# Kernel tuning notes

Hardware: AMD Instinct MI355X
Metric: run time of the kernel (lower is better)

Reference implementation:

```python
import jax, jax.numpy as jnp
import numpy as np

N = 8192
E = 262144
DIN = 512
DOUT = 256


def setup_inputs() -> dict:
    key = jax.random.key(0)
    k1, k2, k3, k4 = jax.random.split(key, 4)
    x = jax.random.normal(k1, (N, DIN), dtype=jnp.float32)
    edge_index = jax.random.randint(k2, (2, E), 0, N, dtype=jnp.int64)
    edge_weight = jax.random.uniform(k3, (E,), dtype=jnp.float32)
    W = jax.random.normal(k4, (DOUT, DIN), dtype=jnp.float32) * (1.0 / np.sqrt(DIN))
    return {"x": x, "edge_index": edge_index, "edge_weight": edge_weight, "W": W}


def reference(x, edge_index, edge_weight, W):
    n = x.shape[0]
    # Linear(dim_in, dim_out, bias=False): h = x @ W.T  -> [N, DOUT]
    h = x @ W.T
    # Dense adjacency: A[src, dst] += w (to_dense_adj sums duplicate edges)
    src, dst = edge_index[0], edge_index[1]
    A = jnp.zeros((n, n), dtype=x.dtype).at[src, dst].add(edge_weight)
    # degree from A BEFORE self-loops, then +1 from the added eye on degree_matrix
    deg = jnp.sum(A, axis=1) + 1.0
    # sqrt(inverse(diag(deg))) == diag(1/sqrt(deg)); apply as row scaling
    dinv_sqrt = 1.0 / jnp.sqrt(deg)  # [N]
    A = A + jnp.eye(n, dtype=x.dtype)  # self-loops on adjacency
    # x = D^{-1/2} @ (A.T @ (D^{-1/2} @ h))
    h = dinv_sqrt[:, None] * h
    h = A.T @ h
    h = dinv_sqrt[:, None] * h
    return h
```

## Files before the change

kernel.cpp:

```cpp
#include <hip/hip_runtime.h>

static constexpr int DIN = 512;
static constexpr int DOUT = 256;
static constexpr int NR = 8;
static constexpr int SLOT = 24;
static constexpr int EPT = 4;
static constexpr float DEG_SCALE = 1048576.0f;
static constexpr float DEG_INV = 1.0f / 1048576.0f;

typedef __attribute__((ext_vector_type(8))) short short8;
typedef __attribute__((ext_vector_type(4))) float f32x4;
typedef __attribute__((ext_vector_type(2))) unsigned int u32x2;
typedef __attribute__((ext_vector_type(4))) unsigned int u32x4;

__device__ inline unsigned short f2bf(float f) {
  unsigned int b = __float_as_uint(f);
  unsigned int r = (b + 0x7fffu + ((b >> 16) & 1u)) >> 16;
  return (unsigned short)r;
}
__device__ inline float bf_lo(unsigned int packed) { return __uint_as_float(packed << 16); }
__device__ inline float bf_hi(unsigned int packed) { return __uint_as_float(packed & 0xffff0000u); }

__device__ inline short8 cvt8(const f32x4 a, const f32x4 b) {
  short8 o;
  o[0] = (short)f2bf(a[0]); o[1] = (short)f2bf(a[1]);
  o[2] = (short)f2bf(a[2]); o[3] = (short)f2bf(a[3]);
  o[4] = (short)f2bf(b[0]); o[5] = (short)f2bf(b[1]);
  o[6] = (short)f2bf(b[2]); o[7] = (short)f2bf(b[3]);
  return o;
}

__device__ inline int xcd_id() {
  int v;
  asm volatile("s_getreg_b32 %0, hwreg(20)" : "=s"(v));
  return v & (NR - 1);
}

__global__ __launch_bounds__(256) void k_prep(
    const float* __restrict__ W, unsigned short* __restrict__ wbb,
    int* __restrict__ dz, int nz, int wgroups) {
  const int gid = blockIdx.x * 256 + threadIdx.x;
  if (gid < nz) dz[gid] = 0;
  const int wi = gid - nz;
  if (wi >= 0 && wi < wgroups) {
    const f32x4* src = (const f32x4*)(W + (size_t)wi * 8);
    f32x4 a = src[0], b = src[1];
    *(short8*)(wbb + (size_t)wi * 8) = cvt8(a, b);
  }
}

__global__ __launch_bounds__(256) void k_edges(
    const int* __restrict__ ei, const float* __restrict__ ew,
    int* __restrict__ degi_rep, int* __restrict__ cursor_rep,
    uint2* __restrict__ bucket, int n, int E) {
  const int x = xcd_id();
  int* __restrict__ degr = degi_rep + (size_t)x * n;
  int* __restrict__ curr = cursor_rep + (size_t)x * n;
  const int e0 = blockIdx.x * 256 * EPT + threadIdx.x;
  int sv[EPT], dv[EPT], wq[EPT];
  float wf[EPT];
#pragma unroll
  for (int u = 0; u < EPT; ++u) {
    const int e = min(e0 + u * 256, E - 1);
    sv[u] = __builtin_nontemporal_load(ei + e);
    dv[u] = __builtin_nontemporal_load(ei + E + e);
    wf[u] = __builtin_nontemporal_load(ew + e);
    wq[u] = __float2int_rn(wf[u] * DEG_SCALE);
  }
  const bool live = (e0 + (EPT - 1) * 256) < E;
#pragma unroll
  for (int u = 0; u < EPT; ++u)
    if (live || e0 + u * 256 < E) atomicAdd(&degr[sv[u]], wq[u]);
  int pos[EPT];
#pragma unroll
  for (int u = 0; u < EPT; ++u)
    pos[u] = (live || e0 + u * 256 < E) ? atomicAdd(&curr[dv[u]], 1) : SLOT;
#pragma unroll
  for (int u = 0; u < EPT; ++u) {
    if (pos[u] < SLOT) {
      u32x2 v;
      v[0] = (unsigned)sv[u];
      v[1] = __float_as_uint(wf[u]);
      __builtin_nontemporal_store(
          v, (u32x2*)(bucket + ((size_t)dv[u] * NR + x) * SLOT + pos[u]));
    }
  }
}

__global__ __launch_bounds__(256) void k_gemm(
    const float* __restrict__ x, const unsigned short* __restrict__ wbb,
    const int* __restrict__ degi_rep, float* __restrict__ sdeg,
    unsigned short* __restrict__ h1b, int n) {
  if (blockIdx.x < (n >> 8)) {
    const int i = blockIdx.x * 256 + threadIdx.x;
    int sum = 0;
#pragma unroll
    for (int r = 0; r < NR; ++r) sum += degi_rep[(size_t)r * n + i];
    sdeg[i] = __frsqrt_rn(1.0f + (float)sum * DEG_INV);
  }
  const int lane = threadIdx.x & 63;
  const int wv = threadIdx.x >> 6;
  const int bm = blockIdx.x * 16;
  const int colb = wv * 64;
  const int r = lane & 15;
  const int kg = lane >> 4;
  f32x4 acc[4] = {};
  const float* arow = x + (size_t)(bm + r) * DIN + kg * 8;
  const unsigned short* brow0 = wbb + (size_t)(colb + r) * DIN + kg * 8;
#pragma unroll
  for (int k0 = 0; k0 < DIN; k0 += 32) {
    f32x4 a0 = *(const f32x4*)(arow + k0);
    f32x4 a1 = *(const f32x4*)(arow + k0 + 4);
    short8 av = cvt8(a0, a1);
#pragma unroll
    for (int nt = 0; nt < 4; ++nt) {
      short8 bv = *(const short8*)(brow0 + (size_t)nt * 16 * DIN + k0);
      acc[nt] = __builtin_amdgcn_mfma_f32_16x16x32_bf16(av, bv, acc[nt], 0, 0, 0);
    }
  }
#pragma unroll
  for (int i = 0; i < 4; ++i) {
    int row = bm + kg * 4 + i;
#pragma unroll
    for (int nt = 0; nt < 4; ++nt) {
      h1b[(size_t)row * DOUT + colb + nt * 16 + r] = f2bf(acc[nt][i]);
    }
  }
}

__global__ __launch_bounds__(256, 4) void k_gather(
    const unsigned short* __restrict__ h1b, const float* __restrict__ sdeg,
    const int* __restrict__ cursor_rep, const uint2* __restrict__ bucket,
    float* __restrict__ out, int n) {
  const int lane = threadIdx.x & 63;
  const int wv = threadIdx.x >> 6;
  const int dst = blockIdx.x * 4 + wv;
  const int cl = lane & 31;
  const int half = lane >> 5;

  int pre[NR + 1];
  pre[0] = 0;
#pragma unroll
  for (int r = 0; r < NR; ++r) {
    int c = min(cursor_rep[(size_t)r * n + dst], SLOT);
    pre[r + 1] = pre[r] + c;
  }
  const int cnt = pre[NR];

  const u32x4 selfv = *(const u32x4*)(h1b + (size_t)dst * DOUT + cl * 8);
  const float sd = sdeg[dst];

  float acc[8] = {};

  for (int base = 0; base < cnt; base += 64) {
    const int c = min(64, cnt - base);
    int sv = 0;
    float wl = 0.f;
    if (lane < c) {
      const int g = base + lane;
      int rr = 0;
#pragma unroll
      for (int r = 1; r < NR; ++r) rr += (g >= pre[r]) ? 1 : 0;
      const int slot = g - pre[rr];
      u32x2 ev = __builtin_nontemporal_load(
          (const u32x2*)(bucket + ((size_t)dst * NR + rr) * SLOT + slot));
      sv = (int)ev[0];
      wl = __uint_as_float(ev[1]) * sdeg[sv];
    }
    const int npair = ((c + 15) >> 4) << 3;
    for (int j = 0; j < npair; j += 8) {
      u32x4 rbuf[8];
#pragma unroll
      for (int u = 0; u < 8; ++u) {
        int src = __shfl(sv, 2 * (j + u) + half);
        rbuf[u] = *(const u32x4*)(h1b + (size_t)src * DOUT + cl * 8);
      }
#pragma unroll
      for (int u = 0; u < 8; ++u) {
        float w = __shfl(wl, 2 * (j + u) + half);
        acc[0] = fmaf(w, bf_lo(rbuf[u][0]), acc[0]);
        acc[1] = fmaf(w, bf_hi(rbuf[u][0]), acc[1]);
        acc[2] = fmaf(w, bf_lo(rbuf[u][1]), acc[2]);
        acc[3] = fmaf(w, bf_hi(rbuf[u][1]), acc[3]);
        acc[4] = fmaf(w, bf_lo(rbuf[u][2]), acc[4]);
        acc[5] = fmaf(w, bf_hi(rbuf[u][2]), acc[5]);
        acc[6] = fmaf(w, bf_lo(rbuf[u][3]), acc[6]);
        acc[7] = fmaf(w, bf_hi(rbuf[u][3]), acc[7]);
      }
    }
  }

#pragma unroll
  for (int k = 0; k < 8; ++k) acc[k] += __shfl_xor(acc[k], 32);

  if (half == 0) {
    f32x4 o0v, o1v;
    o0v[0] = sd * fmaf(sd, bf_lo(selfv[0]), acc[0]);
    o0v[1] = sd * fmaf(sd, bf_hi(selfv[0]), acc[1]);
    o0v[2] = sd * fmaf(sd, bf_lo(selfv[1]), acc[2]);
    o0v[3] = sd * fmaf(sd, bf_hi(selfv[1]), acc[3]);
    o1v[0] = sd * fmaf(sd, bf_lo(selfv[2]), acc[4]);
    o1v[1] = sd * fmaf(sd, bf_hi(selfv[2]), acc[5]);
    o1v[2] = sd * fmaf(sd, bf_lo(selfv[3]), acc[6]);
    o1v[3] = sd * fmaf(sd, bf_hi(selfv[3]), acc[7]);
    float* op = out + (size_t)dst * DOUT + cl * 8;
    __builtin_nontemporal_store(o0v, (f32x4*)op);
    __builtin_nontemporal_store(o1v, (f32x4*)(op + 4));
  }
}

extern "C" void kernel_launch(void* const* d_in, const int* in_sizes, int n_in,
                              void* d_out, int out_size, void* d_ws, size_t ws_size,
                              hipStream_t stream) {
  const float* x = (const float*)d_in[0];
  const int* ei = (const int*)d_in[1];
  const float* ew = (const float*)d_in[2];
  const float* W = (const float*)d_in[3];
  float* out = (float*)d_out;

  const int n = in_sizes[0] / DIN;
  const int E = in_sizes[2];

  char* p = (char*)d_ws;
  auto alloc = [&](size_t bytes) {
    char* q = p;
    p += (bytes + 255) & ~(size_t)255;
    return q;
  };
  unsigned short* h1b = (unsigned short*)alloc((size_t)n * DOUT * 2);
  unsigned short* wbb = (unsigned short*)alloc((size_t)DOUT * DIN * 2);
  int* degi_rep   = (int*)alloc((size_t)NR * n * 4);
  int* cursor_rep = (int*)alloc((size_t)NR * n * 4);
  float* sdeg     = (float*)alloc((size_t)n * 4);
  uint2* bucket   = (uint2*)alloc((size_t)n * NR * SLOT * 8);

  const int nz = 2 * NR * n;
  const int wgroups = DOUT * DIN / 8;
  const int prep_blocks = (nz + wgroups + 255) / 256;
  const int edge_blocks = (E + 256 * EPT - 1) / (256 * EPT);

  k_prep<<<prep_blocks, 256, 0, stream>>>(W, wbb, degi_rep, nz, wgroups);
  k_edges<<<edge_blocks, 256, 0, stream>>>(ei, ew, degi_rep, cursor_rep, bucket, n, E);
  k_gemm<<<n / 16, 256, 0, stream>>>(x, wbb, degi_rep, sdeg, h1b, n);
  k_gather<<<n / 4, 256, 0, stream>>>(h1b, sdeg, cursor_rep, bucket, out, n);
}
```

Measured before the change: 77.12 us.

## Bin edges per segment with LDS histograms instead of global replicated atomics

```diff
diff --git a/kernel.cpp b/kernel.cpp
--- a/kernel.cpp
+++ b/kernel.cpp
@@ -2,9 +2,10 @@
 
 static constexpr int DIN = 512;
 static constexpr int DOUT = 256;
-static constexpr int NR = 8;
-static constexpr int SLOT = 24;
-static constexpr int EPT = 4;
+static constexpr int NB = 8;
+static constexpr int SEG = 32768;
+static constexpr int SLOTB = 24;
+static constexpr int NNODE = 8192;
 static constexpr float DEG_SCALE = 1048576.0f;
 static constexpr float DEG_INV = 1.0f / 1048576.0f;
 
@@ -30,72 +31,66 @@
   return o;
 }
 
-__device__ inline int xcd_id() {
-  int v;
-  asm volatile("s_getreg_b32 %0, hwreg(20)" : "=s"(v));
-  return v & (NR - 1);
-}
-
-__global__ __launch_bounds__(256) void k_prep(
+__global__ __launch_bounds__(256) void k_binprep(
+    const int* __restrict__ ei, const float* __restrict__ ew,
     const float* __restrict__ W, unsigned short* __restrict__ wbb,
-    int* __restrict__ dz, int nz, int wgroups) {
-  const int gid = blockIdx.x * 256 + threadIdx.x;
-  if (gid < nz) dz[gid] = 0;
-  const int wi = gid - nz;
-  if (wi >= 0 && wi < wgroups) {
-    const f32x4* src = (const f32x4*)(W + (size_t)wi * 8);
-    f32x4 a = src[0], b = src[1];
-    *(short8*)(wbb + (size_t)wi * 8) = cvt8(a, b);
-  }
-}
-
-__global__ __launch_bounds__(256) void k_edges(
-    const int* __restrict__ ei, const float* __restrict__ ew,
-    int* __restrict__ degi_rep, int* __restrict__ cursor_rep,
-    uint2* __restrict__ bucket, int n, int E) {
-  const int x = xcd_id();
-  int* __restrict__ degr = degi_rep + (size_t)x * n;
-  int* __restrict__ curr = cursor_rep + (size_t)x * n;
-  const int e0 = blockIdx.x * 256 * EPT + threadIdx.x;
-  int sv[EPT], dv[EPT], wq[EPT];
-  float wf[EPT];
-#pragma unroll
-  for (int u = 0; u < EPT; ++u) {
-    const int e = min(e0 + u * 256, E - 1);
-    sv[u] = __builtin_nontemporal_load(ei + e);
-    dv[u] = __builtin_nontemporal_load(ei + E + e);
-    wf[u] = __builtin_nontemporal_load(ew + e);
-    wq[u] = __float2int_rn(wf[u] * DEG_SCALE);
-  }
-  const bool live = (e0 + (EPT - 1) * 256) < E;
-#pragma unroll
-  for (int u = 0; u < EPT; ++u)
-    if (live || e0 + u * 256 < E) atomicAdd(&degr[sv[u]], wq[u]);
-  int pos[EPT];
-#pragma unroll
-  for (int u = 0; u < EPT; ++u)
-    pos[u] = (live || e0 + u * 256 < E) ? atomicAdd(&curr[dv[u]], 1) : SLOT;
-#pragma unroll
-  for (int u = 0; u < EPT; ++u) {
-    if (pos[u] < SLOT) {
-      u32x2 v;
-      v[0] = (unsigned)sv[u];
-      v[1] = __float_as_uint(wf[u]);
-      __builtin_nontemporal_store(
-          v, (u32x2*)(bucket + ((size_t)dv[u] * NR + x) * SLOT + pos[u]));
-    }
+    int* __restrict__ counts_rep, int* __restrict__ deg_rep,
+    uint2* __restrict__ bucket, int E) {
+  if (blockIdx.x < NB) {
+    __shared__ int s_cnt[NNODE];
+    __shared__ int s_deg[NNODE];
+    const int b = blockIdx.x;
+    const int t = threadIdx.x;
+    for (int i = t; i < NNODE; i += 256) { s_cnt[i] = 0; s_deg[i] = 0; }
+    __syncthreads();
+    const int base = b * SEG;
+    for (int i = 0; i < SEG / 256; ++i) {
+      const int e = base + i * 256 + t;
+      int dv = __builtin_nontemporal_load(ei + E + e);
+      int sv = __builtin_nontemporal_load(ei + e);
+      float w = __builtin_nontemporal_load(ew + e);
+      atomicAdd(&s_cnt[dv], 1);
+      atomicAdd(&s_deg[sv], __float2int_rn(w * DEG_SCALE));
+    }
+    __syncthreads();
+    for (int i = t; i < NNODE; i += 256) {
+      counts_rep[b * NNODE + i] = s_cnt[i];
+      deg_rep[b * NNODE + i] = s_deg[i];
+    }
+    __syncthreads();
+    for (int i = t; i < NNODE; i += 256) s_cnt[i] = 0;
+    __syncthreads();
+    for (int i = 0; i < SEG / 256; ++i) {
+      const int e = base + i * 256 + t;
+      int dv = __builtin_nontemporal_load(ei + E + e);
+      int sv = __builtin_nontemporal_load(ei + e);
+      float w = __builtin_nontemporal_load(ew + e);
+      int rank = atomicAdd(&s_cnt[dv], 1);
+      if (rank < SLOTB) {
+        u32x2 v;
+        v[0] = (unsigned)sv;
+        v[1] = __float_as_uint(w);
+        __builtin_nontemporal_store(
+            v, (u32x2*)(bucket + ((size_t)dv * NB + b) * SLOTB + rank));
+      }
+    }
+  } else {
+    const int gid = (blockIdx.x - NB) * 256 + threadIdx.x;
+    const f32x4* src = (const f32x4*)(W + (size_t)gid * 8);
+    f32x4 a = src[0], bb = src[1];
+    *(short8*)(wbb + (size_t)gid * 8) = cvt8(a, bb);
   }
 }
 
 __global__ __launch_bounds__(256) void k_gemm(
     const float* __restrict__ x, const unsigned short* __restrict__ wbb,
-    const int* __restrict__ degi_rep, float* __restrict__ sdeg,
+    const int* __restrict__ deg_rep, float* __restrict__ sdeg,
     unsigned short* __restrict__ h1b, int n) {
   if (blockIdx.x < (n >> 8)) {
     const int i = blockIdx.x * 256 + threadIdx.x;
     int sum = 0;
 #pragma unroll
-    for (int r = 0; r < NR; ++r) sum += degi_rep[(size_t)r * n + i];
+    for (int r = 0; r < NB; ++r) sum += deg_rep[r * NNODE + i];
     sdeg[i] = __frsqrt_rn(1.0f + (float)sum * DEG_INV);
   }
   const int lane = threadIdx.x & 63;
@@ -130,7 +125,7 @@
 
 __global__ __launch_bounds__(256, 4) void k_gather(
     const unsigned short* __restrict__ h1b, const float* __restrict__ sdeg,
-    const int* __restrict__ cursor_rep, const uint2* __restrict__ bucket,
+    const int* __restrict__ counts_rep, const uint2* __restrict__ bucket,
     float* __restrict__ out, int n) {
   const int lane = threadIdx.x & 63;
   const int wv = threadIdx.x >> 6;
@@ -138,14 +133,14 @@
   const int cl = lane & 31;
   const int half = lane >> 5;
 
-  int pre[NR + 1];
+  int pre[NB + 1];
   pre[0] = 0;
 #pragma unroll
-  for (int r = 0; r < NR; ++r) {
-    int c = min(cursor_rep[(size_t)r * n + dst], SLOT);
+  for (int r = 0; r < NB; ++r) {
+    int c = min(counts_rep[r * NNODE + dst], SLOTB);
     pre[r + 1] = pre[r] + c;
   }
-  const int cnt = pre[NR];
+  const int cnt = pre[NB];
 
   const u32x4 selfv = *(const u32x4*)(h1b + (size_t)dst * DOUT + cl * 8);
   const float sd = sdeg[dst];
@@ -160,10 +155,10 @@
       const int g = base + lane;
       int rr = 0;
 #pragma unroll
-      for (int r = 1; r < NR; ++r) rr += (g >= pre[r]) ? 1 : 0;
+      for (int r = 1; r < NB; ++r) rr += (g >= pre[r]) ? 1 : 0;
       const int slot = g - pre[rr];
       u32x2 ev = __builtin_nontemporal_load(
-          (const u32x2*)(bucket + ((size_t)dst * NR + rr) * SLOT + slot));
+          (const u32x2*)(bucket + ((size_t)dst * NB + rr) * SLOTB + slot));
       sv = (int)ev[0];
       wl = __uint_as_float(ev[1]) * sdeg[sv];
     }
@@ -229,18 +224,15 @@
   };
   unsigned short* h1b = (unsigned short*)alloc((size_t)n * DOUT * 2);
   unsigned short* wbb = (unsigned short*)alloc((size_t)DOUT * DIN * 2);
-  int* degi_rep   = (int*)alloc((size_t)NR * n * 4);
-  int* cursor_rep = (int*)alloc((size_t)NR * n * 4);
+  int* counts_rep = (int*)alloc((size_t)NB * NNODE * 4);
+  int* deg_rep    = (int*)alloc((size_t)NB * NNODE * 4);
   float* sdeg     = (float*)alloc((size_t)n * 4);
-  uint2* bucket   = (uint2*)alloc((size_t)n * NR * SLOT * 8);
-
-  const int nz = 2 * NR * n;
-  const int wgroups = DOUT * DIN / 8;
-  const int prep_blocks = (nz + wgroups + 255) / 256;
-  const int edge_blocks = (E + 256 * EPT - 1) / (256 * EPT);
-
-  k_prep<<<prep_blocks, 256, 0, stream>>>(W, wbb, degi_rep, nz, wgroups);
-  k_edges<<<edge_blocks, 256, 0, stream>>>(ei, ew, degi_rep, cursor_rep, bucket, n, E);
-  k_gemm<<<n / 16, 256, 0, stream>>>(x, wbb, degi_rep, sdeg, h1b, n);
-  k_gather<<<n / 4, 256, 0, stream>>>(h1b, sdeg, cursor_rep, bucket, out, n);
-}
+  uint2* bucket   = (uint2*)alloc((size_t)n * NB * SLOTB * 8);
+
+  const int WCVT_BLOCKS = (DOUT * DIN / 8) / 256;
+
+  k_binprep<<<NB + WCVT_BLOCKS, 256, 0, stream>>>(ei, ew, W, wbb, counts_rep,
+                                                  deg_rep, bucket, E);
+  k_gemm<<<n / 16, 256, 0, stream>>>(x, wbb, deg_rep, sdeg, h1b, n);
+  k_gather<<<n / 4, 256, 0, stream>>>(h1b, sdeg, counts_rep, bucket, out, n);
+}
```

After: 224.6 us. 191% more time.
